# Kernel optimization log

Hardware: AMD Instinct MI355X
Metric: run time of the kernel (lower is better)

Reference implementation:

```python
import jax, jax.numpy as jnp
import numpy as np

NEG_SLOPE = 0.2
EPS = 1e-16


def setup_inputs() -> dict:
    key = jax.random.key(0)
    k = jax.random.split(key, 6)
    N, K, D_IN, D_OUT = 20000, 32, 256, 256
    nodes = jax.random.normal(k[0], (N, D_IN), dtype=jnp.float32)
    neighbors = jax.random.normal(k[1], (N, K, D_IN), dtype=jnp.float32)
    # xavier-uniform-ish scales for faithfulness to init_params
    lim_w = float(np.sqrt(6.0 / (D_IN + D_OUT)))
    W = jax.random.uniform(k[2], (D_OUT, D_IN), minval=-lim_w, maxval=lim_w, dtype=jnp.float32)
    lim_a = float(np.sqrt(6.0 / (1 + D_OUT)))
    a_src = jax.random.uniform(k[3], (D_OUT,), minval=-lim_a, maxval=lim_a, dtype=jnp.float32)
    a_tgt = jax.random.uniform(k[4], (D_OUT,), minval=-lim_a, maxval=lim_a, dtype=jnp.float32)
    bias = jnp.zeros((D_OUT,), dtype=jnp.float32)
    return {"nodes": nodes, "neighbors": neighbors, "W": W, "a_src": a_src, "a_tgt": a_tgt, "bias": bias}


def reference(nodes, neighbors, W, a_src, a_tgt, bias):
    # GAT layer (num_of_heads=1), eval mode (dropout = identity).
    # nodes: [N, D_in], neighbors: [N, K, D_in]
    nodes_proj = nodes @ W.T                              # [N, D_out]
    scores_t = nodes_proj @ a_tgt                         # [N]
    neigh_proj = jnp.einsum('nkf,of->nko', neighbors, W)  # [N, K, D_out]
    scores_s = neigh_proj @ a_src                         # [N, K]
    e = scores_s + scores_t[:, None]                      # per-edge raw score
    e = jnp.where(e >= 0, e, NEG_SLOPE * e)               # leakyReLU(0.2)
    exp_e = jnp.exp(e)                                    # original uses raw exp (no max-subtract)
    attn = exp_e / (jnp.sum(exp_e, axis=1, keepdims=True) + EPS)  # [N, K]
    out = jnp.einsum('nk,nko->no', attn, neigh_proj)      # weighted sum over neighbors
    out = out + bias
    return jax.nn.elu(out)                                # activation = ELU
```

## Files before the change

kernel.cpp:

```cpp
#include <hip/hip_runtime.h>
#include <hip/hip_bf16.h>
#include <math.h>

#define D 256
#define KNB 32
#define NEG_SLOPE 0.2f

using bfrag = __attribute__((ext_vector_type(8))) short;
using ffrag = __attribute__((ext_vector_type(4))) float;

__device__ __forceinline__ unsigned short f2bf(float x) {
    __hip_bfloat16 h = __float2bfloat16(x);
    return *reinterpret_cast<unsigned short*>(&h);
}
__device__ __forceinline__ float bf2f(unsigned short u) {
    return __uint_as_float((unsigned)u << 16);
}

__global__ __launch_bounds__(256) void prep_kernel(
    const float* __restrict__ W, const float* __restrict__ a_src,
    const float* __restrict__ a_tgt, float* __restrict__ ws)
{
    int t = threadIdx.x;
    int b = blockIdx.x;
    if (b < 64) {
        const float4* w4 = reinterpret_cast<const float4*>(W);
        float4 v = w4[b * 256 + t];
        ushort4 u;
        u.x = f2bf(v.x); u.y = f2bf(v.y); u.z = f2bf(v.z); u.w = f2bf(v.w);
        reinterpret_cast<ushort4*>(ws + 512)[b * 256 + t] = u;
    } else {
        float as = 0.f, at = 0.f;
        for (int o = 0; o < D; ++o) {
            float w = W[o * D + t];
            as = fmaf(a_src[o], w, as);
            at = fmaf(a_tgt[o], w, at);
        }
        ws[t]     = as;
        ws[D + t] = at;
    }
}

__global__ __launch_bounds__(256) void attn_agg_kernel(
    const float* __restrict__ nodes, const float* __restrict__ neighbors,
    const float* __restrict__ ws, unsigned short* __restrict__ aggbf, int N)
{
    __shared__ __align__(16) unsigned short sn[KNB][D];
    __shared__ float sp[KNB];

    int t = threadIdx.x;
    int n = blockIdx.x;
    int lane = t & 63, w = t >> 6;

    float4 wsv = reinterpret_cast<const float4*>(ws)[lane];

    float4 nv  = reinterpret_cast<const float4*>(nodes + (size_t)n * D)[lane];
    float4 wtv = reinterpret_cast<const float4*>(ws + D)[lane];
    float st = nv.x * wtv.x + nv.y * wtv.y + nv.z * wtv.z + nv.w * wtv.w;
    #pragma unroll
    for (int o = 1; o < 64; o <<= 1) st += __shfl_xor(st, o);

    const float4* g = reinterpret_cast<const float4*>(neighbors + (size_t)n * (KNB * D));
    float pk[8];
    #pragma unroll
    for (int i = 0; i < 8; ++i) {
        float4 x = g[i * 256 + t];
        ushort4 u;
        u.x = f2bf(x.x); u.y = f2bf(x.y); u.z = f2bf(x.z); u.w = f2bf(x.w);
        *reinterpret_cast<ushort4*>(&sn[i * 4 + w][lane * 4]) = u;
        pk[i] = x.x * wsv.x + x.y * wsv.y + x.z * wsv.z + x.w * wsv.w;
    }
    #pragma unroll
    for (int i = 0; i < 8; ++i) {
        #pragma unroll
        for (int o = 1; o < 64; o <<= 1) pk[i] += __shfl_xor(pk[i], o);
    }
    if (lane == 0) {
        #pragma unroll
        for (int i = 0; i < 8; ++i) {
            float e = pk[i] + st;
            e = (e >= 0.f) ? e : NEG_SLOPE * e;
            sp[i * 4 + w] = __expf(e);
        }
    }
    __syncthreads();

    float sum = 0.f, acc = 0.f;
    #pragma unroll
    for (int k = 0; k < KNB; ++k) {
        float p = sp[k];
        sum += p;
        acc = fmaf(p, bf2f(sn[k][t]), acc);
    }
    aggbf[(size_t)n * D + t] = f2bf(acc / (sum + 1e-16f));
}

__global__ __launch_bounds__(64) void out_gemm_kernel(
    const unsigned short* __restrict__ aggbf,
    const unsigned short* __restrict__ wbf,
    const float* __restrict__ bias, float* __restrict__ out, int N)
{
    int l = threadIdx.x;
    int m0 = blockIdx.x * 16;
    if (m0 >= N) return;
    int lr = l & 15, lk = l >> 4;

    ffrag acc[16];
    #pragma unroll
    for (int nf = 0; nf < 16; ++nf) acc[nf] = ffrag{0.f, 0.f, 0.f, 0.f};

    #pragma unroll
    for (int ks = 0; ks < 8; ++ks) {
        bfrag a = *reinterpret_cast<const bfrag*>(
            aggbf + (size_t)(m0 + lr) * D + ks * 32 + lk * 8);
        #pragma unroll
        for (int nf = 0; nf < 16; ++nf) {
            bfrag b = *reinterpret_cast<const bfrag*>(
                wbf + (size_t)(nf * 16 + lr) * D + ks * 32 + lk * 8);
            acc[nf] = __builtin_amdgcn_mfma_f32_16x16x32_bf16(a, b, acc[nf], 0, 0, 0);
        }
    }

    #pragma unroll
    for (int nf = 0; nf < 16; ++nf) {
        int col = nf * 16 + lr;
        float bv = bias[col];
        #pragma unroll
        for (int r = 0; r < 4; ++r) {
            int m = m0 + lk * 4 + r;
            float x = acc[nf][r] + bv;
            x = (x > 0.f) ? x : expm1f(x);
            out[(size_t)m * D + col] = x;
        }
    }
}

extern "C" void kernel_launch(void* const* d_in, const int* in_sizes, int n_in,
                              void* d_out, int out_size, void* d_ws, size_t ws_size,
                              hipStream_t stream) {
    const float* nodes     = (const float*)d_in[0];
    const float* neighbors = (const float*)d_in[1];
    const float* W         = (const float*)d_in[2];
    const float* a_src     = (const float*)d_in[3];
    const float* a_tgt     = (const float*)d_in[4];
    const float* bias      = (const float*)d_in[5];
    float* out = (float*)d_out;
    float* ws  = (float*)d_ws;

    int N = in_sizes[0] / D;
    unsigned short* wbf   = (unsigned short*)(ws + 512);
    unsigned short* aggbf = (unsigned short*)(ws + 33280);

    hipLaunchKernelGGL(prep_kernel, dim3(65), dim3(256), 0, stream,
                       W, a_src, a_tgt, ws);
    hipLaunchKernelGGL(attn_agg_kernel, dim3(N), dim3(256), 0, stream,
                       nodes, neighbors, ws, aggbf, N);
    hipLaunchKernelGGL(out_gemm_kernel, dim3(N / 16), dim3(64), 0, stream,
                       aggbf, wbf, bias, out, N);
}
```

Before: 189.3 us.

## Make attention aggregation persistent with double-buffered async global-to-LDS neighbor loads

```diff
diff --git a/kernel.cpp b/kernel.cpp
--- a/kernel.cpp
+++ b/kernel.cpp
@@ -5,6 +5,7 @@
 #define D 256
 #define KNB 32
 #define NEG_SLOPE 0.2f
+#define GRID_AGG 512
 
 using bfrag = __attribute__((ext_vector_type(8))) short;
 using ffrag = __attribute__((ext_vector_type(4))) float;
@@ -12,9 +13,6 @@
 __device__ __forceinline__ unsigned short f2bf(float x) {
     __hip_bfloat16 h = __float2bfloat16(x);
     return *reinterpret_cast<unsigned short*>(&h);
-}
-__device__ __forceinline__ float bf2f(unsigned short u) {
-    return __uint_as_float((unsigned)u << 16);
 }
 
 __global__ __launch_bounds__(256) void prep_kernel(
@@ -41,58 +39,117 @@
     }
 }
 
+__global__ __launch_bounds__(256) void scores_t_kernel(
+    const float* __restrict__ nodes, const float* __restrict__ ws,
+    float* __restrict__ scores_t, int N)
+{
+    int wid  = threadIdx.x >> 6;
+    int lane = threadIdx.x & 63;
+    int n = blockIdx.x * 4 + wid;
+    if (n >= N) return;
+    float4 v = reinterpret_cast<const float4*>(nodes + (size_t)n * D)[lane];
+    float4 w = reinterpret_cast<const float4*>(ws + D)[lane];
+    float s = v.x * w.x + v.y * w.y + v.z * w.z + v.w * w.w;
+    #pragma unroll
+    for (int off = 1; off < 64; off <<= 1) s += __shfl_xor(s, off);
+    if (lane == 0) scores_t[n] = s;
+}
+
 __global__ __launch_bounds__(256) void attn_agg_kernel(
-    const float* __restrict__ nodes, const float* __restrict__ neighbors,
-    const float* __restrict__ ws, unsigned short* __restrict__ aggbf, int N)
-{
-    __shared__ __align__(16) unsigned short sn[KNB][D];
+    const float* __restrict__ neighbors, const float* __restrict__ ws,
+    const float* __restrict__ scores_t, unsigned short* __restrict__ aggbf, int N)
+{
+    __shared__ __align__(16) float sn[2][KNB * D];
     __shared__ float sp[KNB];
 
-    int t = threadIdx.x;
-    int n = blockIdx.x;
-    int lane = t & 63, w = t >> 6;
-
-    float4 wsv = reinterpret_cast<const float4*>(ws)[lane];
-
-    float4 nv  = reinterpret_cast<const float4*>(nodes + (size_t)n * D)[lane];
-    float4 wtv = reinterpret_cast<const float4*>(ws + D)[lane];
-    float st = nv.x * wtv.x + nv.y * wtv.y + nv.z * wtv.z + nv.w * wtv.w;
-    #pragma unroll
-    for (int o = 1; o < 64; o <<= 1) st += __shfl_xor(st, o);
-
-    const float4* g = reinterpret_cast<const float4*>(neighbors + (size_t)n * (KNB * D));
-    float pk[8];
-    #pragma unroll
-    for (int i = 0; i < 8; ++i) {
-        float4 x = g[i * 256 + t];
-        ushort4 u;
-        u.x = f2bf(x.x); u.y = f2bf(x.y); u.z = f2bf(x.z); u.w = f2bf(x.w);
-        *reinterpret_cast<ushort4*>(&sn[i * 4 + w][lane * 4]) = u;
-        pk[i] = x.x * wsv.x + x.y * wsv.y + x.z * wsv.z + x.w * wsv.w;
-    }
-    #pragma unroll
-    for (int i = 0; i < 8; ++i) {
-        #pragma unroll
-        for (int o = 1; o < 64; o <<= 1) pk[i] += __shfl_xor(pk[i], o);
-    }
-    if (lane == 0) {
+    const int t    = threadIdx.x;
+    const int lane = t & 63;
+    const int w    = t >> 6;
+    const int b    = blockIdx.x;
+    const int j    = t & 7;
+    const int k    = t >> 3;
+
+    float4 wsv[8];
+    #pragma unroll
+    for (int m = 0; m < 8; ++m)
+        wsv[m] = reinterpret_cast<const float4*>(ws)[j * 8 + m];
+
+    const int nd = (N - 1 - b) / GRID_AGG + 1;
+
+    {
+        const float* gbase = neighbors + (size_t)b * (KNB * D);
         #pragma unroll
         for (int i = 0; i < 8; ++i) {
-            float e = pk[i] + st;
+            int r = i * 4 + w;
+            const float* src = gbase + r * D + ((lane ^ (r & 7)) << 2);
+            __builtin_amdgcn_global_load_lds(
+                (const __attribute__((address_space(1))) void*)src,
+                (__attribute__((address_space(3))) void*)(&sn[0][r * D]),
+                16, 0, 0);
+        }
+    }
+
+    int cur = 0;
+    for (int it = 0; it < nd; ++it) {
+        const int n = b + it * GRID_AGG;
+        const float st = scores_t[n];
+
+        if (it + 1 < nd) {
+            const float* gbase = neighbors + (size_t)(n + GRID_AGG) * (KNB * D);
+            float* dbuf = &sn[cur ^ 1][0];
+            #pragma unroll
+            for (int i = 0; i < 8; ++i) {
+                int r = i * 4 + w;
+                const float* src = gbase + r * D + ((lane ^ (r & 7)) << 2);
+                __builtin_amdgcn_global_load_lds(
+                    (const __attribute__((address_space(1))) void*)src,
+                    (__attribute__((address_space(3))) void*)(dbuf + r * D),
+                    16, 0, 0);
+            }
+            asm volatile("s_waitcnt vmcnt(8)" ::: "memory");
+        } else {
+            asm volatile("s_waitcnt vmcnt(0)" ::: "memory");
+        }
+        __builtin_amdgcn_s_barrier();
+        __builtin_amdgcn_sched_barrier(0);
+
+        const float* buf = &sn[cur][0];
+
+        float p = 0.f;
+        #pragma unroll
+        for (int m = 0; m < 8; ++m) {
+            float4 v = *reinterpret_cast<const float4*>(
+                &buf[k * D + (((j * 8 + m) ^ (k & 7)) << 2)]);
+            p = fmaf(v.x, wsv[m].x,
+                fmaf(v.y, wsv[m].y,
+                fmaf(v.z, wsv[m].z,
+                fmaf(v.w, wsv[m].w, p))));
+        }
+        p += __shfl_xor(p, 1);
+        p += __shfl_xor(p, 2);
+        p += __shfl_xor(p, 4);
+        if (j == 0) {
+            float e = p + st;
             e = (e >= 0.f) ? e : NEG_SLOPE * e;
-            sp[i * 4 + w] = __expf(e);
-        }
-    }
-    __syncthreads();
-
-    float sum = 0.f, acc = 0.f;
-    #pragma unroll
-    for (int k = 0; k < KNB; ++k) {
-        float p = sp[k];
-        sum += p;
-        acc = fmaf(p, bf2f(sn[k][t]), acc);
-    }
-    aggbf[(size_t)n * D + t] = f2bf(acc / (sum + 1e-16f));
+            sp[k] = __expf(e);
+        }
+        asm volatile("s_waitcnt lgkmcnt(0)" ::: "memory");
+        __builtin_amdgcn_s_barrier();
+        __builtin_amdgcn_sched_barrier(0);
+
+        float sum = 0.f, acc = 0.f;
+        #pragma unroll
+        for (int kk = 0; kk < KNB; ++kk) {
+            float pv = sp[kk];
+            sum += pv;
+            acc = fmaf(pv, buf[kk * D + (((t >> 2) ^ (kk & 7)) << 2) + (t & 3)], acc);
+        }
+        aggbf[(size_t)n * D + t] = f2bf(acc / (sum + 1e-16f));
+
+        __builtin_amdgcn_s_barrier();
+        __builtin_amdgcn_sched_barrier(0);
+        cur ^= 1;
+    }
 }
 
 __global__ __launch_bounds__(64) void out_gemm_kernel(
@@ -149,12 +206,15 @@
 
     int N = in_sizes[0] / D;
     unsigned short* wbf   = (unsigned short*)(ws + 512);
-    unsigned short* aggbf = (unsigned short*)(ws + 33280);
+    float* scores_t       = ws + 33280;
+    unsigned short* aggbf = (unsigned short*)(ws + 53280);
 
     hipLaunchKernelGGL(prep_kernel, dim3(65), dim3(256), 0, stream,
                        W, a_src, a_tgt, ws);
-    hipLaunchKernelGGL(attn_agg_kernel, dim3(N), dim3(256), 0, stream,
-                       nodes, neighbors, ws, aggbf, N);
+    hipLaunchKernelGGL(scores_t_kernel, dim3((N + 3) / 4), dim3(256), 0, stream,
+                       nodes, ws, scores_t, N);
+    hipLaunchKernelGGL(attn_agg_kernel, dim3(GRID_AGG), dim3(256), 0, stream,
+                       neighbors, ws, scores_t, aggbf, N);
     hipLaunchKernelGGL(out_gemm_kernel, dim3(N / 16), dim3(64), 0, stream,
                        aggbf, wbf, bias, out, N);
 }
```

Measured after the change: 197.1 us. 4.1% more time.

## Restructure attention aggregation with register-held tiles and split prep reduction

Applied to the files above, without the earlier changes.

```diff
diff --git a/kernel.cpp b/kernel.cpp
--- a/kernel.cpp
+++ b/kernel.cpp
@@ -6,6 +6,9 @@
 #define KNB 32
 #define NEG_SLOPE 0.2f
 
+#define PART_OFF 53280
+#define AGG_OFF  69664
+
 using bfrag = __attribute__((ext_vector_type(8))) short;
 using ffrag = __attribute__((ext_vector_type(4))) float;
 
@@ -13,86 +16,153 @@
     __hip_bfloat16 h = __float2bfloat16(x);
     return *reinterpret_cast<unsigned short*>(&h);
 }
-__device__ __forceinline__ float bf2f(unsigned short u) {
-    return __uint_as_float((unsigned)u << 16);
-}
-
-__global__ __launch_bounds__(256) void prep_kernel(
+
+__global__ __launch_bounds__(256) void prep1_kernel(
     const float* __restrict__ W, const float* __restrict__ a_src,
     const float* __restrict__ a_tgt, float* __restrict__ ws)
 {
     int t = threadIdx.x;
     int b = blockIdx.x;
     if (b < 64) {
-        const float4* w4 = reinterpret_cast<const float4*>(W);
-        float4 v = w4[b * 256 + t];
+        float4 v = reinterpret_cast<const float4*>(W)[b * 256 + t];
         ushort4 u;
         u.x = f2bf(v.x); u.y = f2bf(v.y); u.z = f2bf(v.z); u.w = f2bf(v.w);
         reinterpret_cast<ushort4*>(ws + 512)[b * 256 + t] = u;
     } else {
-        float as = 0.f, at = 0.f;
-        for (int o = 0; o < D; ++o) {
-            float w = W[o * D + t];
-            as = fmaf(a_src[o], w, as);
-            at = fmaf(a_tgt[o], w, at);
+        int bb = b - 64;
+        float ps = 0.f, pt = 0.f;
+        #pragma unroll
+        for (int oo = 0; oo < 8; ++oo) {
+            int o = bb * 8 + oo;
+            float wv = W[o * D + t];
+            ps = fmaf(a_src[o], wv, ps);
+            pt = fmaf(a_tgt[o], wv, pt);
         }
-        ws[t]     = as;
-        ws[D + t] = at;
-    }
+        ws[PART_OFF + bb * 256 + t]        = ps;
+        ws[PART_OFF + 8192 + bb * 256 + t] = pt;
+    }
+}
+
+__global__ __launch_bounds__(256) void prep2_kernel(float* __restrict__ ws)
+{
+    int t = threadIdx.x;
+    float s = 0.f, g = 0.f;
+    #pragma unroll
+    for (int j = 0; j < 32; ++j) {
+        s += ws[PART_OFF + j * 256 + t];
+        g += ws[PART_OFF + 8192 + j * 256 + t];
+    }
+    ws[t]     = s;
+    ws[D + t] = g;
+}
+
+__global__ __launch_bounds__(256) void scores_t_kernel(
+    const float* __restrict__ nodes, const float* __restrict__ ws,
+    float* __restrict__ scores_t, int N)
+{
+    int wid  = threadIdx.x >> 6;
+    int lane = threadIdx.x & 63;
+    int n = blockIdx.x * 4 + wid;
+    if (n >= N) return;
+    float4 v = reinterpret_cast<const float4*>(nodes + (size_t)n * D)[lane];
+    float4 w = reinterpret_cast<const float4*>(ws + D)[lane];
+    float s = v.x * w.x + v.y * w.y + v.z * w.z + v.w * w.w;
+    #pragma unroll
+    for (int off = 1; off < 64; off <<= 1) s += __shfl_xor(s, off);
+    if (lane == 0) scores_t[n] = s;
 }
 
 __global__ __launch_bounds__(256) void attn_agg_kernel(
-    const float* __restrict__ nodes, const float* __restrict__ neighbors,
-    const float* __restrict__ ws, unsigned short* __restrict__ aggbf, int N)
-{
-    __shared__ __align__(16) unsigned short sn[KNB][D];
-    __shared__ float sp[KNB];
-
-    int t = threadIdx.x;
-    int n = blockIdx.x;
-    int lane = t & 63, w = t >> 6;
-
-    float4 wsv = reinterpret_cast<const float4*>(ws)[lane];
-
-    float4 nv  = reinterpret_cast<const float4*>(nodes + (size_t)n * D)[lane];
-    float4 wtv = reinterpret_cast<const float4*>(ws + D)[lane];
-    float st = nv.x * wtv.x + nv.y * wtv.y + nv.z * wtv.z + nv.w * wtv.w;
-    #pragma unroll
-    for (int o = 1; o < 64; o <<= 1) st += __shfl_xor(st, o);
-
-    const float4* g = reinterpret_cast<const float4*>(neighbors + (size_t)n * (KNB * D));
-    float pk[8];
-    #pragma unroll
-    for (int i = 0; i < 8; ++i) {
-        float4 x = g[i * 256 + t];
+    const float* __restrict__ neighbors, const float* __restrict__ ws,
+    const float* __restrict__ scores_t, unsigned short* __restrict__ aggbf, int N)
+{
+    __shared__ __align__(16) float4 part[16][64];
+    __shared__ __align__(16) float4 part2[4][64];
+    __shared__ float wsum[4];
+
+    const int t   = threadIdx.x;
+    const int n   = blockIdx.x;
+    const int w   = t >> 6;
+    const int s   = (t >> 4) & 3;
+    const int c16 = t & 15;
+    const int g   = t >> 4;
+    const int R   = 8 * w + 2 * s;
+
+    const float4* tile = reinterpret_cast<const float4*>(
+        neighbors + (size_t)n * (KNB * D));
+    float4 v[8];
+    #pragma unroll
+    for (int j = 0; j < 8; ++j)
+        v[j] = tile[(R + (j >> 2)) * 64 + (j & 3) * 16 + c16];
+
+    const float4* ws4 = reinterpret_cast<const float4*>(ws);
+    float4 wsv[4];
+    #pragma unroll
+    for (int m = 0; m < 4; ++m) wsv[m] = ws4[m * 16 + c16];
+
+    const float st = scores_t[n];
+
+    float pA = 0.f, pB = 0.f;
+    #pragma unroll
+    for (int m = 0; m < 4; ++m) {
+        pA = fmaf(v[m].x, wsv[m].x, fmaf(v[m].y, wsv[m].y,
+             fmaf(v[m].z, wsv[m].z, fmaf(v[m].w, wsv[m].w, pA))));
+        pB = fmaf(v[4+m].x, wsv[m].x, fmaf(v[4+m].y, wsv[m].y,
+             fmaf(v[4+m].z, wsv[m].z, fmaf(v[4+m].w, wsv[m].w, pB))));
+    }
+    #pragma unroll
+    for (int off = 1; off < 16; off <<= 1) {
+        pA += __shfl_xor(pA, off);
+        pB += __shfl_xor(pB, off);
+    }
+
+    float eA = pA + st; eA = (eA >= 0.f) ? eA : NEG_SLOPE * eA;
+    float eB = pB + st; eB = (eB >= 0.f) ? eB : NEG_SLOPE * eB;
+    float xA = __expf(eA);
+    float xB = __expf(eB);
+
+    float gs = xA + xB;
+    gs += __shfl_xor(gs, 16);
+    gs += __shfl_xor(gs, 32);
+    if ((t & 63) == 0) wsum[w] = gs;
+
+    #pragma unroll
+    for (int m = 0; m < 4; ++m) {
+        float4 a;
+        a.x = fmaf(xA, v[m].x, xB * v[4+m].x);
+        a.y = fmaf(xA, v[m].y, xB * v[4+m].y);
+        a.z = fmaf(xA, v[m].z, xB * v[4+m].z);
+        a.w = fmaf(xA, v[m].w, xB * v[4+m].w);
+        part[g][(m * 16 + c16) ^ ((g & 3) << 1)] = a;
+    }
+    __syncthreads();
+
+    {
+        int q = t & 63, gg = t >> 6;
+        float4 sum = part[gg * 4 + 0][q ^ 0];
+        float4 b1  = part[gg * 4 + 1][q ^ 2];
+        float4 b2  = part[gg * 4 + 2][q ^ 4];
+        float4 b3  = part[gg * 4 + 3][q ^ 6];
+        sum.x += b1.x + b2.x + b3.x;
+        sum.y += b1.y + b2.y + b3.y;
+        sum.z += b1.z + b2.z + b3.z;
+        sum.w += b1.w + b2.w + b3.w;
+        part2[gg][q] = sum;
+    }
+    __syncthreads();
+
+    if (t < 64) {
+        float4 a0 = part2[0][t], a1 = part2[1][t], a2 = part2[2][t], a3 = part2[3][t];
+        float inv = 1.f / (wsum[0] + wsum[1] + wsum[2] + wsum[3] + 1e-16f);
+        float4 r;
+        r.x = (a0.x + a1.x + a2.x + a3.x) * inv;
+        r.y = (a0.y + a1.y + a2.y + a3.y) * inv;
+        r.z = (a0.z + a1.z + a2.z + a3.z) * inv;
+        r.w = (a0.w + a1.w + a2.w + a3.w) * inv;
         ushort4 u;
-        u.x = f2bf(x.x); u.y = f2bf(x.y); u.z = f2bf(x.z); u.w = f2bf(x.w);
-        *reinterpret_cast<ushort4*>(&sn[i * 4 + w][lane * 4]) = u;
-        pk[i] = x.x * wsv.x + x.y * wsv.y + x.z * wsv.z + x.w * wsv.w;
-    }
-    #pragma unroll
-    for (int i = 0; i < 8; ++i) {
-        #pragma unroll
-        for (int o = 1; o < 64; o <<= 1) pk[i] += __shfl_xor(pk[i], o);
-    }
-    if (lane == 0) {
-        #pragma unroll
-        for (int i = 0; i < 8; ++i) {
-            float e = pk[i] + st;
-            e = (e >= 0.f) ? e : NEG_SLOPE * e;
-            sp[i * 4 + w] = __expf(e);
-        }
-    }
-    __syncthreads();
-
-    float sum = 0.f, acc = 0.f;
-    #pragma unroll
-    for (int k = 0; k < KNB; ++k) {
-        float p = sp[k];
-        sum += p;
-        acc = fmaf(p, bf2f(sn[k][t]), acc);
-    }
-    aggbf[(size_t)n * D + t] = f2bf(acc / (sum + 1e-16f));
+        u.x = f2bf(r.x); u.y = f2bf(r.y); u.z = f2bf(r.z); u.w = f2bf(r.w);
+        reinterpret_cast<ushort4*>(aggbf + (size_t)n * D)[t] = u;
+    }
 }
 
 __global__ __launch_bounds__(64) void out_gemm_kernel(
@@ -149,12 +219,16 @@
 
     int N = in_sizes[0] / D;
     unsigned short* wbf   = (unsigned short*)(ws + 512);
-    unsigned short* aggbf = (unsigned short*)(ws + 33280);
-
-    hipLaunchKernelGGL(prep_kernel, dim3(65), dim3(256), 0, stream,
+    float* scores_t       = ws + 33280;
+    unsigned short* aggbf = (unsigned short*)(ws + AGG_OFF);
+
+    hipLaunchKernelGGL(prep1_kernel, dim3(96), dim3(256), 0, stream,
                        W, a_src, a_tgt, ws);
+    hipLaunchKernelGGL(prep2_kernel, dim3(1), dim3(256), 0, stream, ws);
+    hipLaunchKernelGGL(scores_t_kernel, dim3((N + 3) / 4), dim3(256), 0, stream,
+                       nodes, ws, scores_t, N);
     hipLaunchKernelGGL(attn_agg_kernel, dim3(N), dim3(256), 0, stream,
-                       nodes, neighbors, ws, aggbf, N);
+                       neighbors, ws, scores_t, aggbf, N);
     hipLaunchKernelGGL(out_gemm_kernel, dim3(N / 16), dim3(64), 0, stream,
                        aggbf, wbf, bias, out, N);
 }
```

Result: no change. 185.9 us (-1.8%).
